# Performance work log

Measured on AMD Instinct MI355X. Metric: run time of the kernel, lower is better.

Reference implementation:

```python
import jax, jax.numpy as jnp
import numpy as np

N_NODES = 100000


def _gcn_conv(x, W, b, src, dst, deg_inv_sqrt):
    # linear transform first (PyG GCNConv order): [N, F] @ [F, H]
    h = x @ W
    # symmetric normalization per edge: deg^-1/2[src] * deg^-1/2[dst]
    norm = deg_inv_sqrt[src] * deg_inv_sqrt[dst]
    msg = h[src] * norm[:, None]  # [E, H]
    out = jax.ops.segment_sum(msg, dst, num_segments=N_NODES)
    return out + b


def setup_inputs() -> dict:
    key = jax.random.key(0)
    k1, k2, k3, k4 = jax.random.split(key, 4)
    F_IN, H = 512, 512
    E = 800000
    x = jax.random.normal(k1, (N_NODES, F_IN), dtype=jnp.float32)
    edge_index = jax.random.randint(k2, (2, E), 0, N_NODES, dtype=jnp.int64)
    W1 = jax.random.normal(k3, (F_IN, H), dtype=jnp.float32) * (1.0 / np.sqrt(F_IN))
    b1 = jnp.zeros((H,), dtype=jnp.float32)
    W2 = jax.random.normal(k4, (H, H), dtype=jnp.float32) * (1.0 / np.sqrt(H))
    b2 = jnp.zeros((H,), dtype=jnp.float32)
    return {"x": x, "edge_index": edge_index, "W1": W1, "b1": b1, "W2": W2, "b2": b2}


def reference(x, edge_index, W1, b1, W2, b2):
    # add self loops (PyG GCNConv default add_self_loops=True)
    loop = jnp.arange(N_NODES, dtype=edge_index.dtype)
    src = jnp.concatenate([edge_index[0], loop])
    dst = jnp.concatenate([edge_index[1], loop])
    # degree of destination nodes (including self loops)
    deg = jax.ops.segment_sum(jnp.ones_like(dst, dtype=x.dtype), dst, num_segments=N_NODES)
    deg_inv_sqrt = jnp.where(deg > 0, jax.lax.rsqrt(jnp.maximum(deg, 1.0)), 0.0)
    h = jax.nn.relu(_gcn_conv(x, W1, b1, src, dst, deg_inv_sqrt))
    # dropout is identity at inference (training=False)
    out = _gcn_conv(h, W2, b2, src, dst, deg_inv_sqrt)
    return out
```

## Files before the change

kernel.cpp:

```cpp
#include <hip/hip_runtime.h>

#define N_NODES 100000
#define E_EDGES 800000
#define E_TOT   900000
#define F 512

typedef __attribute__((ext_vector_type(8))) short short8;
typedef __attribute__((ext_vector_type(4))) float f32x4;
typedef unsigned int u32;

__device__ __forceinline__ float bfu(unsigned int u) {
    union { unsigned int i; float f; } c; c.i = u << 16; return c.f;
}
__device__ __forceinline__ unsigned short f2b(float f) {
    union { float f; unsigned int u; } c; c.f = f;
    return (unsigned short)((c.u + 0x7fffu + ((c.u >> 16) & 1u)) >> 16);
}
__device__ __forceinline__ float fbits(unsigned int u) {
    union { unsigned int i; float f; } c; c.i = u; return c.f;
}
__device__ __forceinline__ unsigned int bits(float f) {
    union { float f; unsigned int i; } c; c.f = f; return c.i;
}
__device__ __forceinline__ void gload_lds16(const void* g, void* l) {
    __builtin_amdgcn_global_load_lds(
        (const __attribute__((address_space(1))) u32*)g,
        (__attribute__((address_space(3))) u32*)l, 16, 0, 0);
}

__global__ void k_init(unsigned int* deg, unsigned int* counter) {
    int i = blockIdx.x * 256 + threadIdx.x;
    if (i < N_NODES) deg[i] = 1u;
    if (i == 0) *counter = 0u;
}

__global__ void k_hist(const int* __restrict__ ei, unsigned int* deg) {
    int e = blockIdx.x * 256 + threadIdx.x;
    if (e < E_EDGES) atomicAdd(&deg[ei[E_EDGES + e]], 1u);
}

__global__ void k_dis(const unsigned int* __restrict__ deg, float* __restrict__ dis) {
    int i = blockIdx.x * 256 + threadIdx.x;
    if (i < N_NODES) dis[i] = rsqrtf((float)deg[i]);
}

__global__ void k_alloc(const unsigned int* __restrict__ deg, unsigned int* counter,
                        int2* __restrict__ seg, unsigned int* __restrict__ cursor) {
    int i = blockIdx.x * 256 + threadIdx.x;
    if (i < N_NODES) {
        unsigned int d = deg[i];
        unsigned int p = atomicAdd(counter, d);
        seg[i] = make_int2((int)p, (int)(p + d));
        cursor[i] = p;
    }
}

__global__ void k_scatter(const int* __restrict__ ei, const float* __restrict__ dis,
                          unsigned int* __restrict__ cursor,
                          uint2* __restrict__ ev) {
    int e = blockIdx.x * 256 + threadIdx.x;
    if (e < E_TOT) {
        int s, d;
        if (e < E_EDGES) { s = ei[e]; d = ei[E_EDGES + e]; }
        else             { s = e - E_EDGES; d = s; }
        unsigned int p = atomicAdd(&cursor[d], 1u);
        ev[p] = make_uint2((unsigned)s, bits(dis[s] * dis[d]));
    }
}

__global__ void k_cvtX(const float* __restrict__ xin, unsigned short* __restrict__ xb) {
    int i = blockIdx.x * 256 + threadIdx.x;
    const float4* p = (const float4*)xin + (size_t)i * 2;
    float4 a = p[0], b = p[1];
    uint4 o;
    o.x = (unsigned)f2b(a.x) | ((unsigned)f2b(a.y) << 16);
    o.y = (unsigned)f2b(a.z) | ((unsigned)f2b(a.w) << 16);
    o.z = (unsigned)f2b(b.x) | ((unsigned)f2b(b.y) << 16);
    o.w = (unsigned)f2b(b.z) | ((unsigned)f2b(b.w) << 16);
    *(uint4*)(xb + (size_t)i * 8) = o;
}

__global__ void k_cvtW(const float* __restrict__ W, unsigned short* __restrict__ Wt) {
    int t = blockIdx.x * 256 + threadIdx.x;
    if (t < F * F) {
        int n = t >> 9, k = t & 511;
        Wt[t] = f2b(W[k * F + n]);
    }
}

__global__ __launch_bounds__(256)
void gemm_bt(const unsigned short* __restrict__ A, const unsigned short* __restrict__ Bt,
             const float* __restrict__ bias,
             unsigned short* __restrict__ outb, float* __restrict__ outf,
             int relu, int M) {
    __shared__ unsigned short lsa[128 * 64];
    __shared__ unsigned short lsb[128 * 64];
    int bx = blockIdx.x;
    int by = blockIdx.y;
    int t  = threadIdx.x;
    int lane = t & 63, w = t >> 6;
    int wr = w >> 1, wc = w & 1;

    f32x4 acc[4][4];
    #pragma unroll
    for (int m = 0; m < 4; ++m)
        #pragma unroll
        for (int n = 0; n < 4; ++n)
            acc[m][n] = (f32x4){0.f, 0.f, 0.f, 0.f};

    int rowBase = bx * 128;

    int ar[4], akc[4], br[4];
    #pragma unroll
    for (int i = 0; i < 4; ++i) {
        int idx = i * 256 + t;
        int r = idx >> 3;
        akc[i] = (idx & 7) * 8;
        int ga = rowBase + r; if (ga >= M) ga = M - 1;
        ar[i] = ga;
        br[i] = by * 128 + r;
    }

    for (int k0 = 0; k0 < F; k0 += 64) {
        #pragma unroll
        for (int i = 0; i < 4; ++i) {
            int idx = i * 256 + t;
            gload_lds16(A + (size_t)ar[i] * F + k0 + akc[i], lsa + idx * 8);
            gload_lds16(Bt + (size_t)br[i] * F + k0 + akc[i], lsb + idx * 8);
        }
        __syncthreads();
        #pragma unroll
        for (int ks = 0; ks < 2; ++ks) {
            int koff = ks * 32 + (lane >> 4) * 8;
            short8 af[4], bfr[4];
            #pragma unroll
            for (int m = 0; m < 4; ++m)
                af[m] = *(short8*)&lsa[(wr * 64 + m * 16 + (lane & 15)) * 64 + koff];
            #pragma unroll
            for (int n = 0; n < 4; ++n)
                bfr[n] = *(short8*)&lsb[(wc * 64 + n * 16 + (lane & 15)) * 64 + koff];
            #pragma unroll
            for (int m = 0; m < 4; ++m)
                #pragma unroll
                for (int n = 0; n < 4; ++n)
                    acc[m][n] = __builtin_amdgcn_mfma_f32_16x16x32_bf16(af[m], bfr[n], acc[m][n], 0, 0, 0);
        }
        __syncthreads();
    }

    int rq = (lane >> 4) * 4, cq = lane & 15;
    #pragma unroll
    for (int m = 0; m < 4; ++m)
        #pragma unroll
        for (int n = 0; n < 4; ++n) {
            int colv = by * 128 + wc * 64 + n * 16 + cq;
            float bv = bias[colv];
            #pragma unroll
            for (int j = 0; j < 4; ++j) {
                int row = rowBase + wr * 64 + m * 16 + rq + j;
                if (row < M) {
                    float v = acc[m][n][j] + bv;
                    if (relu) v = fmaxf(v, 0.f);
                    if (outb) outb[(size_t)row * F + colv] = f2b(v);
                    else __builtin_nontemporal_store(v, outf + (size_t)row * F + colv);
                }
            }
        }
}

__global__ __launch_bounds__(256)
void k_agg(const unsigned short* __restrict__ hin, const int2* __restrict__ seg,
           const uint2* __restrict__ ev,
           unsigned short* __restrict__ outb) {
    int node = blockIdx.x * 4 + (threadIdx.x >> 6);
    int lane = threadIdx.x & 63;
    if (node >= N_NODES) return;
    int2 se = seg[node];
    int e0 = se.x, e1 = se.y;
    float acc[8] = {0, 0, 0, 0, 0, 0, 0, 0};
    const unsigned short* base = hin + lane * 8;

    int e = e0;
    for (; e + 3 < e1; e += 4) {
        uint2 p0 = ev[e], p1 = ev[e + 1], p2 = ev[e + 2], p3 = ev[e + 3];
        uint4 v0 = *(const uint4*)(base + ((size_t)p0.x << 9));
        uint4 v1 = *(const uint4*)(base + ((size_t)p1.x << 9));
        uint4 v2 = *(const uint4*)(base + ((size_t)p2.x << 9));
        uint4 v3 = *(const uint4*)(base + ((size_t)p3.x << 9));
        float w0 = fbits(p0.y), w1 = fbits(p1.y), w2 = fbits(p2.y), w3 = fbits(p3.y);
        acc[0] += w0 * bfu(v0.x & 0xffffu); acc[1] += w0 * bfu(v0.x >> 16);
        acc[2] += w0 * bfu(v0.y & 0xffffu); acc[3] += w0 * bfu(v0.y >> 16);
        acc[4] += w0 * bfu(v0.z & 0xffffu); acc[5] += w0 * bfu(v0.z >> 16);
        acc[6] += w0 * bfu(v0.w & 0xffffu); acc[7] += w0 * bfu(v0.w >> 16);
        acc[0] += w1 * bfu(v1.x & 0xffffu); acc[1] += w1 * bfu(v1.x >> 16);
        acc[2] += w1 * bfu(v1.y & 0xffffu); acc[3] += w1 * bfu(v1.y >> 16);
        acc[4] += w1 * bfu(v1.z & 0xffffu); acc[5] += w1 * bfu(v1.z >> 16);
        acc[6] += w1 * bfu(v1.w & 0xffffu); acc[7] += w1 * bfu(v1.w >> 16);
        acc[0] += w2 * bfu(v2.x & 0xffffu); acc[1] += w2 * bfu(v2.x >> 16);
        acc[2] += w2 * bfu(v2.y & 0xffffu); acc[3] += w2 * bfu(v2.y >> 16);
        acc[4] += w2 * bfu(v2.z & 0xffffu); acc[5] += w2 * bfu(v2.z >> 16);
        acc[6] += w2 * bfu(v2.w & 0xffffu); acc[7] += w2 * bfu(v2.w >> 16);
        acc[0] += w3 * bfu(v3.x & 0xffffu); acc[1] += w3 * bfu(v3.x >> 16);
        acc[2] += w3 * bfu(v3.y & 0xffffu); acc[3] += w3 * bfu(v3.y >> 16);
        acc[4] += w3 * bfu(v3.z & 0xffffu); acc[5] += w3 * bfu(v3.z >> 16);
        acc[6] += w3 * bfu(v3.w & 0xffffu); acc[7] += w3 * bfu(v3.w >> 16);
    }
    for (; e < e1; ++e) {
        uint2 p = ev[e];
        uint4 v = *(const uint4*)(base + ((size_t)p.x << 9));
        float wv = fbits(p.y);
        acc[0] += wv * bfu(v.x & 0xffffu); acc[1] += wv * bfu(v.x >> 16);
        acc[2] += wv * bfu(v.y & 0xffffu); acc[3] += wv * bfu(v.y >> 16);
        acc[4] += wv * bfu(v.z & 0xffffu); acc[5] += wv * bfu(v.z >> 16);
        acc[6] += wv * bfu(v.w & 0xffffu); acc[7] += wv * bfu(v.w >> 16);
    }

    uint4 o;
    o.x = (unsigned)f2b(acc[0]) | ((unsigned)f2b(acc[1]) << 16);
    o.y = (unsigned)f2b(acc[2]) | ((unsigned)f2b(acc[3]) << 16);
    o.z = (unsigned)f2b(acc[4]) | ((unsigned)f2b(acc[5]) << 16);
    o.w = (unsigned)f2b(acc[6]) | ((unsigned)f2b(acc[7]) << 16);
    *(uint4*)(outb + (size_t)node * F + lane * 8) = o;
}

extern "C" void kernel_launch(void* const* d_in, const int* in_sizes, int n_in,
                              void* d_out, int out_size, void* d_ws, size_t ws_size,
                              hipStream_t stream) {
    const float* x  = (const float*)d_in[0];
    const int*   ei = (const int*)d_in[1];
    const float* W1 = (const float*)d_in[2];
    const float* b1 = (const float*)d_in[3];
    const float* W2 = (const float*)d_in[4];
    const float* b2 = (const float*)d_in[5];
    float* out = (float*)d_out;

    char* ws = (char*)d_ws;
    size_t off = 0;
    auto alloc = [&](size_t bytes) -> void* {
        off = (off + 255) & ~(size_t)255;
        void* p = ws + off;
        off += bytes;
        return p;
    };

    unsigned short* tb  = (unsigned short*)alloc((size_t)N_NODES * F * 2);
    unsigned short* W1t = (unsigned short*)alloc((size_t)F * F * 2);
    unsigned short* W2t = (unsigned short*)alloc((size_t)F * F * 2);
    unsigned int*   deg = (unsigned int*)alloc((size_t)N_NODES * 4);
    float*          dis = (float*)alloc((size_t)N_NODES * 4);
    int2*           seg = (int2*)alloc((size_t)N_NODES * 8);
    unsigned int*   cur = (unsigned int*)alloc((size_t)N_NODES * 4);
    unsigned int*   cnt = (unsigned int*)alloc(256);
    uint2*          ev  = (uint2*)alloc((size_t)E_TOT * 8);

    unsigned short* h1b = (unsigned short*)d_out;
    unsigned short* xb  = (unsigned short*)((char*)d_out + (size_t)N_NODES * F * 2);

    int nb = (N_NODES + 255) / 256;

    k_init<<<nb, 256, 0, stream>>>(deg, cnt);
    k_hist<<<(E_EDGES + 255) / 256, 256, 0, stream>>>(ei, deg);
    k_dis<<<nb, 256, 0, stream>>>(deg, dis);
    k_alloc<<<nb, 256, 0, stream>>>(deg, cnt, seg, cur);
    k_scatter<<<(E_TOT + 255) / 256, 256, 0, stream>>>(ei, dis, cur, ev);

    k_cvtW<<<(F * F + 255) / 256, 256, 0, stream>>>(W1, W1t);
    k_cvtW<<<(F * F + 255) / 256, 256, 0, stream>>>(W2, W2t);
    k_cvtX<<<(N_NODES * F / 8) / 256, 256, 0, stream>>>(x, xb);

    dim3 ggrid((N_NODES + 127) / 128, F / 128);

    k_agg<<<(N_NODES + 3) / 4, 256, 0, stream>>>(xb, seg, ev, tb);
    gemm_bt<<<ggrid, 256, 0, stream>>>(tb, W1t, b1, h1b, nullptr, 1, N_NODES);

    k_agg<<<(N_NODES + 3) / 4, 256, 0, stream>>>(h1b, seg, ev, tb);
    gemm_bt<<<ggrid, 256, 0, stream>>>(tb, W2t, b2, nullptr, out, 0, N_NODES);
}
```

Measured before the change: 723.9 us.

## Double-buffer GEMM LDS tiles and merge small preprocessing kernels

New measurement: 685.2 us. -5.3%, faster.

```diff
diff --git a/kernel.cpp b/kernel.cpp
--- a/kernel.cpp
+++ b/kernel.cpp
@@ -39,16 +39,13 @@
     if (e < E_EDGES) atomicAdd(&deg[ei[E_EDGES + e]], 1u);
 }
 
-__global__ void k_dis(const unsigned int* __restrict__ deg, float* __restrict__ dis) {
-    int i = blockIdx.x * 256 + threadIdx.x;
-    if (i < N_NODES) dis[i] = rsqrtf((float)deg[i]);
-}
-
-__global__ void k_alloc(const unsigned int* __restrict__ deg, unsigned int* counter,
-                        int2* __restrict__ seg, unsigned int* __restrict__ cursor) {
+__global__ void k_disalloc(const unsigned int* __restrict__ deg, unsigned int* counter,
+                           float* __restrict__ dis,
+                           int2* __restrict__ seg, unsigned int* __restrict__ cursor) {
     int i = blockIdx.x * 256 + threadIdx.x;
     if (i < N_NODES) {
         unsigned int d = deg[i];
+        dis[i] = rsqrtf((float)d);
         unsigned int p = atomicAdd(counter, d);
         seg[i] = make_int2((int)p, (int)(p + d));
         cursor[i] = p;
@@ -70,22 +67,26 @@
 
 __global__ void k_cvtX(const float* __restrict__ xin, unsigned short* __restrict__ xb) {
     int i = blockIdx.x * 256 + threadIdx.x;
-    const float4* p = (const float4*)xin + (size_t)i * 2;
-    float4 a = p[0], b = p[1];
+    const f32x4* p = (const f32x4*)xin + (size_t)i * 2;
+    f32x4 a = __builtin_nontemporal_load(p);
+    f32x4 b = __builtin_nontemporal_load(p + 1);
     uint4 o;
-    o.x = (unsigned)f2b(a.x) | ((unsigned)f2b(a.y) << 16);
-    o.y = (unsigned)f2b(a.z) | ((unsigned)f2b(a.w) << 16);
-    o.z = (unsigned)f2b(b.x) | ((unsigned)f2b(b.y) << 16);
-    o.w = (unsigned)f2b(b.z) | ((unsigned)f2b(b.w) << 16);
+    o.x = (unsigned)f2b(a[0]) | ((unsigned)f2b(a[1]) << 16);
+    o.y = (unsigned)f2b(a[2]) | ((unsigned)f2b(a[3]) << 16);
+    o.z = (unsigned)f2b(b[0]) | ((unsigned)f2b(b[1]) << 16);
+    o.w = (unsigned)f2b(b[2]) | ((unsigned)f2b(b[3]) << 16);
     *(uint4*)(xb + (size_t)i * 8) = o;
 }
 
-__global__ void k_cvtW(const float* __restrict__ W, unsigned short* __restrict__ Wt) {
+__global__ void k_cvtW(const float* __restrict__ W1, const float* __restrict__ W2,
+                       unsigned short* __restrict__ W1t, unsigned short* __restrict__ W2t) {
     int t = blockIdx.x * 256 + threadIdx.x;
-    if (t < F * F) {
-        int n = t >> 9, k = t & 511;
-        Wt[t] = f2b(W[k * F + n]);
-    }
+    int which = t >= F * F;
+    int u = t - which * F * F;
+    int n = u >> 9, k = u & 511;
+    const float* W = which ? W2 : W1;
+    unsigned short* Wt = which ? W2t : W1t;
+    Wt[u] = f2b(W[k * F + n]);
 }
 
 __global__ __launch_bounds__(256)
@@ -93,8 +94,8 @@
              const float* __restrict__ bias,
              unsigned short* __restrict__ outb, float* __restrict__ outf,
              int relu, int M) {
-    __shared__ unsigned short lsa[128 * 64];
-    __shared__ unsigned short lsb[128 * 64];
+    __shared__ unsigned short lsa[2][128 * 32];
+    __shared__ unsigned short lsb[2][128 * 32];
     int bx = blockIdx.x;
     int by = blockIdx.y;
     int t  = threadIdx.x;
@@ -110,41 +111,51 @@
 
     int rowBase = bx * 128;
 
-    int ar[4], akc[4], br[4];
-    #pragma unroll
-    for (int i = 0; i < 4; ++i) {
+    int ar[2], br[2], akc[2];
+    #pragma unroll
+    for (int i = 0; i < 2; ++i) {
         int idx = i * 256 + t;
-        int r = idx >> 3;
-        akc[i] = (idx & 7) * 8;
+        int r = idx >> 2;
+        akc[i] = (idx & 3) * 8;
         int ga = rowBase + r; if (ga >= M) ga = M - 1;
         ar[i] = ga;
         br[i] = by * 128 + r;
     }
 
-    for (int k0 = 0; k0 < F; k0 += 64) {
-        #pragma unroll
-        for (int i = 0; i < 4; ++i) {
+    auto STAGE = [&](int buf, int k0) {
+        #pragma unroll
+        for (int i = 0; i < 2; ++i) {
             int idx = i * 256 + t;
-            gload_lds16(A + (size_t)ar[i] * F + k0 + akc[i], lsa + idx * 8);
-            gload_lds16(Bt + (size_t)br[i] * F + k0 + akc[i], lsb + idx * 8);
+            gload_lds16(A + (size_t)ar[i] * F + k0 + akc[i], &lsa[buf][idx * 8]);
+            gload_lds16(Bt + (size_t)br[i] * F + k0 + akc[i], &lsb[buf][idx * 8]);
         }
-        __syncthreads();
-        #pragma unroll
-        for (int ks = 0; ks < 2; ++ks) {
-            int koff = ks * 32 + (lane >> 4) * 8;
-            short8 af[4], bfr[4];
-            #pragma unroll
-            for (int m = 0; m < 4; ++m)
-                af[m] = *(short8*)&lsa[(wr * 64 + m * 16 + (lane & 15)) * 64 + koff];
+    };
+    auto COMPUTE = [&](int buf) {
+        int koff = (lane >> 4) * 8;
+        int rsel = lane & 15;
+        short8 af[4], bfr[4];
+        #pragma unroll
+        for (int m = 0; m < 4; ++m)
+            af[m] = *(short8*)&lsa[buf][(wr * 64 + m * 16 + rsel) * 32 + koff];
+        #pragma unroll
+        for (int n = 0; n < 4; ++n)
+            bfr[n] = *(short8*)&lsb[buf][(wc * 64 + n * 16 + rsel) * 32 + koff];
+        #pragma unroll
+        for (int m = 0; m < 4; ++m)
             #pragma unroll
             for (int n = 0; n < 4; ++n)
-                bfr[n] = *(short8*)&lsb[(wc * 64 + n * 16 + (lane & 15)) * 64 + koff];
-            #pragma unroll
-            for (int m = 0; m < 4; ++m)
-                #pragma unroll
-                for (int n = 0; n < 4; ++n)
-                    acc[m][n] = __builtin_amdgcn_mfma_f32_16x16x32_bf16(af[m], bfr[n], acc[m][n], 0, 0, 0);
-        }
+                acc[m][n] = __builtin_amdgcn_mfma_f32_16x16x32_bf16(af[m], bfr[n], acc[m][n], 0, 0, 0);
+    };
+
+    STAGE(0, 0);
+    __syncthreads();
+    #pragma unroll
+    for (int kp = 0; kp < 8; ++kp) {
+        STAGE(1, (2 * kp + 1) * 32);
+        COMPUTE(0);
+        __syncthreads();
+        if (kp < 7) STAGE(0, (2 * kp + 2) * 32);
+        COMPUTE(1);
         __syncthreads();
     }
 
@@ -260,12 +271,10 @@
 
     k_init<<<nb, 256, 0, stream>>>(deg, cnt);
     k_hist<<<(E_EDGES + 255) / 256, 256, 0, stream>>>(ei, deg);
-    k_dis<<<nb, 256, 0, stream>>>(deg, dis);
-    k_alloc<<<nb, 256, 0, stream>>>(deg, cnt, seg, cur);
+    k_disalloc<<<nb, 256, 0, stream>>>(deg, cnt, dis, seg, cur);
     k_scatter<<<(E_TOT + 255) / 256, 256, 0, stream>>>(ei, dis, cur, ev);
 
-    k_cvtW<<<(F * F + 255) / 256, 256, 0, stream>>>(W1, W1t);
-    k_cvtW<<<(F * F + 255) / 256, 256, 0, stream>>>(W2, W2t);
+    k_cvtW<<<(2 * F * F) / 256, 256, 0, stream>>>(W1, W2, W1t, W2t);
     k_cvtX<<<(N_NODES * F / 8) / 256, 256, 0, stream>>>(x, xb);
 
     dim3 ggrid((N_NODES + 127) / 128, F / 128);
```
